# Optimization experiments

Measured on AMD Instinct MI355X. Metric: run time of the kernel, lower is better.

Reference implementation:

```python
import jax, jax.numpy as jnp
import numpy as np

N_NODES = 100000
N_EDGES = 1600000
IN_DIM = 128
HEADS = 4
OUT_DIM = 32
NEG_SLOPE = 0.2  # PyG GATConv default negative_slope


def setup_inputs() -> dict:
    key = jax.random.key(0)
    k_x, k_e, k_w, k_as, k_ad = jax.random.split(key, 5)
    x = jax.random.normal(k_x, (N_NODES, IN_DIM), dtype=jnp.float32)
    edge_index = jax.random.randint(k_e, (2, N_EDGES), 0, N_NODES, dtype=jnp.int64)
    # Glorot-style init for learned parameters (GATConv lin + attention vectors)
    W = jax.random.normal(k_w, (IN_DIM, HEADS * OUT_DIM), dtype=jnp.float32) / np.sqrt(IN_DIM)
    att_src = jax.random.normal(k_as, (HEADS, OUT_DIM), dtype=jnp.float32) / np.sqrt(OUT_DIM)
    att_dst = jax.random.normal(k_ad, (HEADS, OUT_DIM), dtype=jnp.float32) / np.sqrt(OUT_DIM)
    bias = jnp.zeros((HEADS * OUT_DIM,), dtype=jnp.float32)
    return {"x": x, "edge_index": edge_index, "W": W, "att_src": att_src,
            "att_dst": att_dst, "bias": bias}


def reference(x, edge_index, W, att_src, att_dst, bias):
    N = x.shape[0]
    H, D = att_src.shape
    # PyG GATConv default: add self loops
    loop = jnp.arange(N, dtype=edge_index.dtype)
    src = jnp.concatenate([edge_index[0], loop])  # message sources  [E+N]
    dst = jnp.concatenate([edge_index[1], loop])  # message targets  [E+N]

    h = (x @ W).reshape(N, H, D)                          # [N, H, D]
    a_src = jnp.einsum('nhd,hd->nh', h, att_src)          # [N, H]
    a_dst = jnp.einsum('nhd,hd->nh', h, att_dst)          # [N, H]

    # per-edge attention logits, LeakyReLU(neg_slope=0.2)
    e = jax.nn.leaky_relu(a_src[src] + a_dst[dst], NEG_SLOPE)  # [E+N, H]

    # segment softmax over edges grouped by target node (numerically stable)
    e_max = jax.ops.segment_max(e, dst, num_segments=N)        # [N, H]
    e_max = jnp.where(jnp.isfinite(e_max), e_max, jnp.float32(0))
    ex = jnp.exp(e - e_max[dst])                               # [E+N, H]
    denom = jax.ops.segment_sum(ex, dst, num_segments=N)       # [N, H]
    alpha = ex / (denom[dst] + jnp.float32(1e-16))             # [E+N, H]

    # weighted scatter-aggregate of source features
    msg = h[src] * alpha[:, :, None]                           # [E+N, H, D]
    out = jax.ops.segment_sum(msg, dst, num_segments=N)        # [N, H, D]
    out = out.reshape(N, H * D) + bias                         # concat heads + bias
    return jax.nn.elu(out)                                     # wrapper ELU
```

## Files before the change

kernel.cpp:

```cpp
#include <hip/hip_runtime.h>
#include <hip/hip_fp16.h>
#include <math.h>

#define N_NODES 100000
#define N_EDGES 1600000
#define IN_DIM 128
#define F_DIM 128
#define NEG_SLOPE 0.2f

#define BUCKW_LOG 7
#define NBUCK 784
#define NBLK 128
#define EPB 12500
#define G_TOT (NBUCK * NBLK)
#define SC_CHUNK 4096
#define SC_NB ((G_TOT + SC_CHUNK - 1) / SC_CHUNK)
#define CSR_CAP (N_EDGES + NBUCK * 384)
#define PADBIT 0x80000000u

typedef short v8s __attribute__((ext_vector_type(8)));
typedef float v4f __attribute__((ext_vector_type(4)));

static __device__ __forceinline__ unsigned short f2bf(float f) {
    unsigned u = __float_as_uint(f);
    u += 0x7fffu + ((u >> 16) & 1u);
    return (unsigned short)(u >> 16);
}
static __device__ __forceinline__ float lo2f(unsigned u) { return __uint_as_float(u << 16); }
static __device__ __forceinline__ float hi2f(unsigned u) { return __uint_as_float(u & 0xffff0000u); }

__global__ __launch_bounds__(256) void k_wprep(const float* __restrict__ W,
                                               unsigned short* __restrict__ Wt) {
    int i = blockIdx.x * 256 + threadIdx.x;
    int n = i >> 7, k = i & 127;
    Wt[n * 128 + k] = f2bf(W[k * 128 + n]);
}

__global__ __launch_bounds__(256) void k_gemm(const float* __restrict__ x,
                                              const unsigned short* __restrict__ Wt,
                                              unsigned short* __restrict__ h16,
                                              const float* __restrict__ att_src,
                                              const float* __restrict__ att_dst,
                                              float* __restrict__ a_src,
                                              float* __restrict__ a_dst) {
    __shared__ unsigned short As[64][136];
    __shared__ unsigned short Bs[128][136];
    __shared__ float attl[256];
    const int t  = threadIdx.x;
    const int n0 = blockIdx.x * 64;

    attl[t] = (t < 128) ? att_src[t] : att_dst[t - 128];

    {
        int row = t >> 2, k0 = (t & 3) * 32;
        int n = n0 + row;
        #pragma unroll
        for (int i = 0; i < 4; i++) {
            float4 va = make_float4(0.f,0.f,0.f,0.f), vb = va;
            if (n < N_NODES) {
                const float* p = x + (size_t)n * IN_DIM + k0 + i * 8;
                va = *(const float4*)p;
                vb = *(const float4*)(p + 4);
            }
            uint4 u;
            u.x = f2bf(va.x) | ((unsigned)f2bf(va.y) << 16);
            u.y = f2bf(va.z) | ((unsigned)f2bf(va.w) << 16);
            u.z = f2bf(vb.x) | ((unsigned)f2bf(vb.y) << 16);
            u.w = f2bf(vb.z) | ((unsigned)f2bf(vb.w) << 16);
            *(uint4*)&As[row][k0 + i * 8] = u;
        }
    }
    {
        int nr = t >> 1, s0 = (t & 1) * 64;
        const uint4* src = (const uint4*)(Wt + nr * 128 + s0);
        #pragma unroll
        for (int i = 0; i < 8; i++)
            *(uint4*)&Bs[nr][s0 + i * 8] = src[i];
    }
    __syncthreads();

    const int w = t >> 6, lane = t & 63;
    const int mr = lane & 15, quad = lane >> 4;
    const int m0 = w * 16;

    v4f acc[8];
    #pragma unroll
    for (int nt = 0; nt < 8; nt++) acc[nt] = (v4f){0.f, 0.f, 0.f, 0.f};

    #pragma unroll
    for (int kk = 0; kk < 4; kk++) {
        int kof = kk * 32 + quad * 8;
        v8s a = *(const v8s*)&As[m0 + mr][kof];
        #pragma unroll
        for (int nt = 0; nt < 8; nt++) {
            v8s b = *(const v8s*)&Bs[nt * 16 + mr][kof];
            acc[nt] = __builtin_amdgcn_mfma_f32_16x16x32_bf16(a, b, acc[nt], 0, 0, 0);
        }
    }

    #pragma unroll
    for (int nt = 0; nt < 8; nt++)
        #pragma unroll
        for (int r = 0; r < 4; r++)
            As[m0 + quad * 4 + r][nt * 16 + mr] = f2bf(acc[nt][r]);
    __syncthreads();
    {
        int row = m0 + (lane >> 2);
        int c0  = (lane & 3) * 32;
        int n = n0 + row;
        if (n < N_NODES) {
            float ds = 0.f, dd = 0.f;
            #pragma unroll
            for (int i = 0; i < 4; i++) {
                uint4 v = *(const uint4*)&As[row][c0 + i * 8];
                *(uint4*)&h16[(size_t)n * F_DIM + c0 + i * 8] = v;
                float f0 = lo2f(v.x), f1 = hi2f(v.x);
                float f2 = lo2f(v.y), f3 = hi2f(v.y);
                float f4 = lo2f(v.z), f5 = hi2f(v.z);
                float f6 = lo2f(v.w), f7 = hi2f(v.w);
                const float* ps = &attl[c0 + i * 8];
                const float* pd = &attl[128 + c0 + i * 8];
                ds += f0*ps[0] + f1*ps[1] + f2*ps[2] + f3*ps[3]
                    + f4*ps[4] + f5*ps[5] + f6*ps[6] + f7*ps[7];
                dd += f0*pd[0] + f1*pd[1] + f2*pd[2] + f3*pd[3]
                    + f4*pd[4] + f5*pd[5] + f6*pd[6] + f7*pd[7];
            }
            int hd = lane & 3;
            a_src[n * 4 + hd] = ds;
            a_dst[n * 4 + hd] = dd;
        }
    }
}

__global__ __launch_bounds__(1024) void k_bhist(const int* __restrict__ ei_dst,
                                                int* __restrict__ G) {
    __shared__ int hist[NBUCK];
    for (int i = threadIdx.x; i < NBUCK; i += 1024) hist[i] = 0;
    __syncthreads();
    const int4* p = (const int4*)(ei_dst + blockIdx.x * EPB);
    const int n4 = EPB / 4;
    for (int i = threadIdx.x; i < n4; i += 1024) {
        int4 d = p[i];
        atomicAdd(&hist[d.x >> BUCKW_LOG], 1);
        atomicAdd(&hist[d.y >> BUCKW_LOG], 1);
        atomicAdd(&hist[d.z >> BUCKW_LOG], 1);
        atomicAdd(&hist[d.w >> BUCKW_LOG], 1);
    }
    __syncthreads();
    for (int b = threadIdx.x; b < NBUCK; b += 1024)
        G[b * NBLK + blockIdx.x] = hist[b];
}

__global__ __launch_bounds__(256) void k_scanp(const int* __restrict__ a,
                                               int* __restrict__ part) {
    int base = blockIdx.x * SC_CHUNK + threadIdx.x * 16;
    int s = 0;
    #pragma unroll
    for (int i = 0; i < 16; i++) {
        int idx = base + i;
        if (idx < G_TOT) s += a[idx];
    }
    __shared__ int wsum[4];
    for (int off = 32; off >= 1; off >>= 1) s += __shfl_down(s, off, 64);
    if ((threadIdx.x & 63) == 0) wsum[threadIdx.x >> 6] = s;
    __syncthreads();
    if (threadIdx.x == 0) part[blockIdx.x] = wsum[0] + wsum[1] + wsum[2] + wsum[3];
}

__global__ void k_scant(int* part, int* boff) {
    int lane = threadIdx.x & 63;
    int v = (lane < SC_NB) ? part[lane] : 0;
    int x = v;
    #pragma unroll
    for (int off = 1; off < 64; off <<= 1) {
        int y = __shfl_up(x, off, 64);
        if (lane >= off) x += y;
    }
    if (lane < SC_NB) part[lane] = x - v;
    if (lane == 0) boff[NBUCK] = N_EDGES;
}

__global__ __launch_bounds__(256) void k_scand(int* __restrict__ a,
                                               const int* __restrict__ part,
                                               int* __restrict__ boff) {
    __shared__ int tsum[256];
    int tid  = threadIdx.x;
    int base = blockIdx.x * SC_CHUNK + tid * 16;
    int v[16]; int s = 0;
    #pragma unroll
    for (int i = 0; i < 16; i++) {
        int idx = base + i;
        v[i] = (idx < G_TOT) ? a[idx] : 0;
        s += v[i];
    }
    tsum[tid] = s;
    __syncthreads();
    for (int off = 1; off < 256; off <<= 1) {
        int y = (tid >= off) ? tsum[tid - off] : 0;
        __syncthreads();
        tsum[tid] += y;
        __syncthreads();
    }
    int run = part[blockIdx.x] + tsum[tid] - s;
    #pragma unroll
    for (int i = 0; i < 16; i++) {
        int idx = base + i;
        if (idx < G_TOT) {
            a[idx] = run;
            if (idx % NBLK == 0) boff[idx / NBLK] = run;
        }
        run += v[i];
    }
}

__global__ __launch_bounds__(1024) void k_bscat(const int* __restrict__ ei,
                                                const int* __restrict__ G,
                                                int* __restrict__ ebuf) {
    __shared__ int base[NBUCK];
    for (int b = threadIdx.x; b < NBUCK; b += 1024)
        base[b] = G[b * NBLK + blockIdx.x];
    __syncthreads();
    const int4* ps = (const int4*)(ei + blockIdx.x * EPB);
    const int4* pd = (const int4*)(ei + N_EDGES + blockIdx.x * EPB);
    const int n4 = EPB / 4;
    for (int i = threadIdx.x; i < n4; i += 1024) {
        int4 s = ps[i];
        int4 d = pd[i];
        int b0 = d.x >> BUCKW_LOG; int p0 = atomicAdd(&base[b0], 1);
        ebuf[p0] = s.x | ((d.x & 127) << 17);
        int b1 = d.y >> BUCKW_LOG; int p1 = atomicAdd(&base[b1], 1);
        ebuf[p1] = s.y | ((d.y & 127) << 17);
        int b2 = d.z >> BUCKW_LOG; int p2 = atomicAdd(&base[b2], 1);
        ebuf[p2] = s.z | ((d.z & 127) << 17);
        int b3 = d.w >> BUCKW_LOG; int p3 = atomicAdd(&base[b3], 1);
        ebuf[p3] = s.w | ((d.w & 127) << 17);
    }
}

__global__ __launch_bounds__(512) void k_csrfin(const int* __restrict__ ebuf,
                                                const int* __restrict__ boff,
                                                int2* __restrict__ ebounds,
                                                int* __restrict__ csr2) {
    __shared__ int cnt[128];
    __shared__ int off[128];
    __shared__ int wtot;
    int b = blockIdx.x;
    int beg = boff[b], end = boff[b + 1];
    int padded_base = beg + b * 384;
    int tid = threadIdx.x;
    if (tid < 128) cnt[tid] = 0;
    __syncthreads();
    {
        int j = beg + tid;
        for (; j + 3 * 512 < end; j += 4 * 512) {
            int e0 = ebuf[j];
            int e1 = ebuf[j + 512];
            int e2 = ebuf[j + 1024];
            int e3 = ebuf[j + 1536];
            atomicAdd(&cnt[(e0 >> 17) & 127], 1);
            atomicAdd(&cnt[(e1 >> 17) & 127], 1);
            atomicAdd(&cnt[(e2 >> 17) & 127], 1);
            atomicAdd(&cnt[(e3 >> 17) & 127], 1);
        }
        for (; j < end; j += 512)
            atomicAdd(&cnt[(ebuf[j] >> 17) & 127], 1);
    }
    __syncthreads();
    if (tid < 128) {
        int cp = (cnt[tid] + 3) & ~3;
        int x = cp;
        #pragma unroll
        for (int o = 1; o < 64; o <<= 1) {
            int y = __shfl_up(x, o, 64);
            if ((tid & 63) >= o) x += y;
        }
        off[tid] = x - cp;
        if (tid == 63) wtot = x;
    }
    __syncthreads();
    if (tid < 128) {
        int v = off[tid] + ((tid >= 64) ? wtot : 0) + padded_base;
        off[tid] = v;
        int node = (b << BUCKW_LOG) + tid;
        int c = cnt[tid];
        if (node < N_NODES) {
            ebounds[node] = make_int2(v, v + c);
            int cpad = (c + 3) & ~3;
            for (int k = c; k < cpad; k++)
                csr2[v + k] = node | PADBIT;
        }
        cnt[tid] = 0;
    }
    __syncthreads();
    {
        int j = beg + tid;
        for (; j + 3 * 512 < end; j += 4 * 512) {
            int e0 = ebuf[j];
            int e1 = ebuf[j + 512];
            int e2 = ebuf[j + 1024];
            int e3 = ebuf[j + 1536];
            int d0 = (e0 >> 17) & 127; int r0 = atomicAdd(&cnt[d0], 1);
            csr2[off[d0] + r0] = e0 & 0x1ffff;
            int d1 = (e1 >> 17) & 127; int r1 = atomicAdd(&cnt[d1], 1);
            csr2[off[d1] + r1] = e1 & 0x1ffff;
            int d2 = (e2 >> 17) & 127; int r2 = atomicAdd(&cnt[d2], 1);
            csr2[off[d2] + r2] = e2 & 0x1ffff;
            int d3 = (e3 >> 17) & 127; int r3 = atomicAdd(&cnt[d3], 1);
            csr2[off[d3] + r3] = e3 & 0x1ffff;
        }
        for (; j < end; j += 512) {
            int e0 = ebuf[j];
            int d0 = (e0 >> 17) & 127; int r0 = atomicAdd(&cnt[d0], 1);
            csr2[off[d0] + r0] = e0 & 0x1ffff;
        }
    }
}

__global__ __launch_bounds__(256) void k_agg(const uint4* __restrict__ h16x4,
                                             const float* __restrict__ a_src,
                                             const float* __restrict__ a_dst,
                                             const int2* __restrict__ ebounds,
                                             const int* __restrict__ csr2,
                                             const float* __restrict__ bias,
                                             float* __restrict__ out) {
    int n = (blockIdx.x * 256 + threadIdx.x) >> 6;
    if (n >= N_NODES) return;
    int lane = threadIdx.x & 63;
    int grp = lane >> 4, g = lane & 15, hd = g >> 2;

    float adn = a_dst[n * 4 + hd];
    float p0 = 0.f;
    if (grp == 0) {
        float e0 = a_src[n * 4 + hd] + adn;
        e0 = e0 > 0.f ? e0 : NEG_SLOPE * e0;
        p0 = __expf(e0);
    }
    uint4 hs = h16x4[(size_t)n * 16 + g];
    float l  = p0;
    float a0 = p0 * lo2f(hs.x), a1 = p0 * hi2f(hs.x);
    float a2 = p0 * lo2f(hs.y), a3 = p0 * hi2f(hs.y);
    float a4 = p0 * lo2f(hs.z), a5 = p0 * hi2f(hs.z);
    float a6 = p0 * lo2f(hs.w), a7 = p0 * hi2f(hs.w);

    int2 eb = ebounds[n];
    int beg = eb.x, cnt = eb.y - eb.x;
    const int* sp = csr2 + beg + grp;
    int steps = (cnt + 3) >> 2;
    int t = 0;
    for (; t + 2 <= steps; t += 2) {
        int u0 = sp[4 * t];
        int u1 = sp[4 * t + 4];
        int s0 = u0 & 0x7fffffff;
        int s1 = u1 & 0x7fffffff;
        float w0 = a_src[s0 * 4 + hd] + adn;
        float w1 = a_src[s1 * 4 + hd] + adn;
        uint4 h0 = h16x4[(size_t)s0 * 16 + g];
        uint4 h1 = h16x4[(size_t)s1 * 16 + g];
        w0 = w0 > 0.f ? w0 : NEG_SLOPE * w0;
        w1 = w1 > 0.f ? w1 : NEG_SLOPE * w1;
        float q0 = __expf(w0);
        float q1 = __expf(w1);
        q0 = u0 < 0 ? 0.f : q0;
        q1 = u1 < 0 ? 0.f : q1;
        l  += q0 + q1;
        a0 += q0 * lo2f(h0.x) + q1 * lo2f(h1.x);
        a1 += q0 * hi2f(h0.x) + q1 * hi2f(h1.x);
        a2 += q0 * lo2f(h0.y) + q1 * lo2f(h1.y);
        a3 += q0 * hi2f(h0.y) + q1 * hi2f(h1.y);
        a4 += q0 * lo2f(h0.z) + q1 * lo2f(h1.z);
        a5 += q0 * hi2f(h0.z) + q1 * hi2f(h1.z);
        a6 += q0 * lo2f(h0.w) + q1 * lo2f(h1.w);
        a7 += q0 * hi2f(h0.w) + q1 * hi2f(h1.w);
    }
    if (t < steps) {
        int u0 = sp[4 * t];
        int s0 = u0 & 0x7fffffff;
        float w0 = a_src[s0 * 4 + hd] + adn;
        uint4 h0 = h16x4[(size_t)s0 * 16 + g];
        w0 = w0 > 0.f ? w0 : NEG_SLOPE * w0;
        float q0 = __expf(w0);
        q0 = u0 < 0 ? 0.f : q0;
        l  += q0;
        a0 += q0 * lo2f(h0.x);
        a1 += q0 * hi2f(h0.x);
        a2 += q0 * lo2f(h0.y);
        a3 += q0 * hi2f(h0.y);
        a4 += q0 * lo2f(h0.z);
        a5 += q0 * hi2f(h0.z);
        a6 += q0 * lo2f(h0.w);
        a7 += q0 * hi2f(h0.w);
    }
    #define RED2(v) v += __shfl_xor(v, 16, 64); v += __shfl_xor(v, 32, 64);
    RED2(l); RED2(a0); RED2(a1); RED2(a2); RED2(a3);
    RED2(a4); RED2(a5); RED2(a6); RED2(a7);
    #undef RED2

    if (grp == 0) {
        float inv = 1.f / (l + 1e-16f);
        float4 b0 = *(const float4*)&bias[g * 8];
        float4 b1 = *(const float4*)&bias[g * 8 + 4];
        float o0 = a0 * inv + b0.x, o1 = a1 * inv + b0.y;
        float o2 = a2 * inv + b0.z, o3 = a3 * inv + b0.w;
        float o4 = a4 * inv + b1.x, o5 = a5 * inv + b1.y;
        float o6 = a6 * inv + b1.z, o7 = a7 * inv + b1.w;
        o0 = o0 > 0.f ? o0 : __expf(o0) - 1.f;
        o1 = o1 > 0.f ? o1 : __expf(o1) - 1.f;
        o2 = o2 > 0.f ? o2 : __expf(o2) - 1.f;
        o3 = o3 > 0.f ? o3 : __expf(o3) - 1.f;
        o4 = o4 > 0.f ? o4 : __expf(o4) - 1.f;
        o5 = o5 > 0.f ? o5 : __expf(o5) - 1.f;
        o6 = o6 > 0.f ? o6 : __expf(o6) - 1.f;
        o7 = o7 > 0.f ? o7 : __expf(o7) - 1.f;
        *(float4*)&out[(size_t)n * F_DIM + g * 8]     = make_float4(o0, o1, o2, o3);
        *(float4*)&out[(size_t)n * F_DIM + g * 8 + 4] = make_float4(o4, o5, o6, o7);
    }
}

extern "C" void kernel_launch(void* const* d_in, const int* in_sizes, int n_in,
                              void* d_out, int out_size, void* d_ws, size_t ws_size,
                              hipStream_t stream) {
    const float* x       = (const float*)d_in[0];
    const int*   ei      = (const int*)d_in[1];
    const float* W       = (const float*)d_in[2];
    const float* att_src = (const float*)d_in[3];
    const float* att_dst = (const float*)d_in[4];
    const float* bias    = (const float*)d_in[5];
    float*       out     = (float*)d_out;

    char* ws = (char*)d_ws;
    unsigned short* h16 = (unsigned short*)ws; ws += (size_t)N_NODES * F_DIM * 2;
    unsigned short* Wt  = (unsigned short*)ws; ws += (size_t)IN_DIM * F_DIM * 2;
    float* a_src  = (float*)ws; ws += (size_t)N_NODES * 4 * 4;
    float* a_dst  = (float*)ws; ws += (size_t)N_NODES * 4 * 4;
    int*   G      = (int*)ws;   ws += (size_t)G_TOT * 4;
    int*   part   = (int*)ws;   ws += 1024;
    int*   boff   = (int*)ws;   ws += 4096;
    int2*  ebounds= (int2*)ws;  ws += (size_t)N_NODES * 8 + 512;
    int*   ebuf   = (int*)ws;   ws += (size_t)N_EDGES * 4;
    int*   csr2   = (int*)ws;   ws += (size_t)CSR_CAP * 4;

    k_wprep<<<64, 256, 0, stream>>>(W, Wt);
    k_gemm<<<(N_NODES + 63) / 64, 256, 0, stream>>>(x, Wt, h16, att_src, att_dst, a_src, a_dst);

    k_bhist<<<NBLK, 1024, 0, stream>>>(ei + N_EDGES, G);
    k_scanp<<<SC_NB, 256, 0, stream>>>(G, part);
    k_scant<<<1, 64, 0, stream>>>(part, boff);
    k_scand<<<SC_NB, 256, 0, stream>>>(G, part, boff);
    k_bscat<<<NBLK, 1024, 0, stream>>>(ei, G, ebuf);
    k_csrfin<<<NBUCK, 512, 0, stream>>>(ebuf, boff, ebounds, csr2);

    k_agg<<<(N_NODES * 64 + 255) / 256, 256, 0, stream>>>((const uint4*)h16, a_src, a_dst, ebounds, csr2, bias, out);
}
```

Baseline: 255.4 us.

## Merge GEMM with bucket scatter and fold W prep into histogram kernel

```diff
diff --git a/kernel.cpp b/kernel.cpp
--- a/kernel.cpp
+++ b/kernel.cpp
@@ -17,6 +17,7 @@
 #define SC_NB ((G_TOT + SC_CHUNK - 1) / SC_CHUNK)
 #define CSR_CAP (N_EDGES + NBUCK * 384)
 #define PADBIT 0x80000000u
+#define GB 1563
 
 typedef short v8s __attribute__((ext_vector_type(8)));
 typedef float v4f __attribute__((ext_vector_type(4)));
@@ -29,20 +30,127 @@
 static __device__ __forceinline__ float lo2f(unsigned u) { return __uint_as_float(u << 16); }
 static __device__ __forceinline__ float hi2f(unsigned u) { return __uint_as_float(u & 0xffff0000u); }
 
-__global__ __launch_bounds__(256) void k_wprep(const float* __restrict__ W,
-                                               unsigned short* __restrict__ Wt) {
-    int i = blockIdx.x * 256 + threadIdx.x;
-    int n = i >> 7, k = i & 127;
-    Wt[n * 128 + k] = f2bf(W[k * 128 + n]);
-}
-
-__global__ __launch_bounds__(256) void k_gemm(const float* __restrict__ x,
+__global__ __launch_bounds__(1024) void k_bhist(const int* __restrict__ ei_dst,
+                                                int* __restrict__ G,
+                                                const float* __restrict__ W,
+                                                unsigned short* __restrict__ Wt) {
+    if (blockIdx.x < 16) {
+        int i = blockIdx.x * 1024 + threadIdx.x;
+        int n = i >> 7, k = i & 127;
+        Wt[n * 128 + k] = f2bf(W[k * 128 + n]);
+    }
+    __shared__ int hist[NBUCK];
+    for (int i = threadIdx.x; i < NBUCK; i += 1024) hist[i] = 0;
+    __syncthreads();
+    const int4* p = (const int4*)(ei_dst + blockIdx.x * EPB);
+    const int n4 = EPB / 4;
+    for (int i = threadIdx.x; i < n4; i += 1024) {
+        int4 d = p[i];
+        atomicAdd(&hist[d.x >> BUCKW_LOG], 1);
+        atomicAdd(&hist[d.y >> BUCKW_LOG], 1);
+        atomicAdd(&hist[d.z >> BUCKW_LOG], 1);
+        atomicAdd(&hist[d.w >> BUCKW_LOG], 1);
+    }
+    __syncthreads();
+    for (int b = threadIdx.x; b < NBUCK; b += 1024)
+        G[b * NBLK + blockIdx.x] = hist[b];
+}
+
+__global__ __launch_bounds__(256) void k_scanp(const int* __restrict__ a,
+                                               int* __restrict__ part) {
+    int base = blockIdx.x * SC_CHUNK + threadIdx.x * 16;
+    int s = 0;
+    #pragma unroll
+    for (int i = 0; i < 16; i++) {
+        int idx = base + i;
+        if (idx < G_TOT) s += a[idx];
+    }
+    __shared__ int wsum[4];
+    for (int off = 32; off >= 1; off >>= 1) s += __shfl_down(s, off, 64);
+    if ((threadIdx.x & 63) == 0) wsum[threadIdx.x >> 6] = s;
+    __syncthreads();
+    if (threadIdx.x == 0) part[blockIdx.x] = wsum[0] + wsum[1] + wsum[2] + wsum[3];
+}
+
+__global__ void k_scant(int* part, int* boff) {
+    int lane = threadIdx.x & 63;
+    int v = (lane < SC_NB) ? part[lane] : 0;
+    int x = v;
+    #pragma unroll
+    for (int off = 1; off < 64; off <<= 1) {
+        int y = __shfl_up(x, off, 64);
+        if (lane >= off) x += y;
+    }
+    if (lane < SC_NB) part[lane] = x - v;
+    if (lane == 0) boff[NBUCK] = N_EDGES;
+}
+
+__global__ __launch_bounds__(256) void k_scand(int* __restrict__ a,
+                                               const int* __restrict__ part,
+                                               int* __restrict__ boff) {
+    __shared__ int tsum[256];
+    int tid  = threadIdx.x;
+    int base = blockIdx.x * SC_CHUNK + tid * 16;
+    int v[16]; int s = 0;
+    #pragma unroll
+    for (int i = 0; i < 16; i++) {
+        int idx = base + i;
+        v[i] = (idx < G_TOT) ? a[idx] : 0;
+        s += v[i];
+    }
+    tsum[tid] = s;
+    __syncthreads();
+    for (int off = 1; off < 256; off <<= 1) {
+        int y = (tid >= off) ? tsum[tid - off] : 0;
+        __syncthreads();
+        tsum[tid] += y;
+        __syncthreads();
+    }
+    int run = part[blockIdx.x] + tsum[tid] - s;
+    #pragma unroll
+    for (int i = 0; i < 16; i++) {
+        int idx = base + i;
+        if (idx < G_TOT) {
+            a[idx] = run;
+            if (idx % NBLK == 0) boff[idx / NBLK] = run;
+        }
+        run += v[i];
+    }
+}
+
+__global__ __launch_bounds__(256) void k_mega(const float* __restrict__ x,
                                               const unsigned short* __restrict__ Wt,
                                               unsigned short* __restrict__ h16,
                                               const float* __restrict__ att_src,
                                               const float* __restrict__ att_dst,
                                               float* __restrict__ a_src,
-                                              float* __restrict__ a_dst) {
+                                              float* __restrict__ a_dst,
+                                              const int* __restrict__ ei,
+                                              const int* __restrict__ G,
+                                              int* __restrict__ ebuf) {
+    if (blockIdx.x >= GB) {
+        int blk = blockIdx.x - GB;
+        __shared__ int base[NBUCK];
+        for (int b = threadIdx.x; b < NBUCK; b += 256)
+            base[b] = G[b * NBLK + blk];
+        __syncthreads();
+        const int4* ps = (const int4*)(ei + blk * EPB);
+        const int4* pd = (const int4*)(ei + N_EDGES + blk * EPB);
+        for (int i = threadIdx.x; i < EPB / 4; i += 256) {
+            int4 s = ps[i];
+            int4 d = pd[i];
+            int b0 = d.x >> BUCKW_LOG; int p0 = atomicAdd(&base[b0], 1);
+            ebuf[p0] = s.x | ((d.x & 127) << 17);
+            int b1 = d.y >> BUCKW_LOG; int p1 = atomicAdd(&base[b1], 1);
+            ebuf[p1] = s.y | ((d.y & 127) << 17);
+            int b2 = d.z >> BUCKW_LOG; int p2 = atomicAdd(&base[b2], 1);
+            ebuf[p2] = s.z | ((d.z & 127) << 17);
+            int b3 = d.w >> BUCKW_LOG; int p3 = atomicAdd(&base[b3], 1);
+            ebuf[p3] = s.w | ((d.w & 127) << 17);
+        }
+        return;
+    }
+
     __shared__ unsigned short As[64][136];
     __shared__ unsigned short Bs[128][136];
     __shared__ float attl[256];
@@ -132,111 +240,6 @@
     }
 }
 
-__global__ __launch_bounds__(1024) void k_bhist(const int* __restrict__ ei_dst,
-                                                int* __restrict__ G) {
-    __shared__ int hist[NBUCK];
-    for (int i = threadIdx.x; i < NBUCK; i += 1024) hist[i] = 0;
-    __syncthreads();
-    const int4* p = (const int4*)(ei_dst + blockIdx.x * EPB);
-    const int n4 = EPB / 4;
-    for (int i = threadIdx.x; i < n4; i += 1024) {
-        int4 d = p[i];
-        atomicAdd(&hist[d.x >> BUCKW_LOG], 1);
-        atomicAdd(&hist[d.y >> BUCKW_LOG], 1);
-        atomicAdd(&hist[d.z >> BUCKW_LOG], 1);
-        atomicAdd(&hist[d.w >> BUCKW_LOG], 1);
-    }
-    __syncthreads();
-    for (int b = threadIdx.x; b < NBUCK; b += 1024)
-        G[b * NBLK + blockIdx.x] = hist[b];
-}
-
-__global__ __launch_bounds__(256) void k_scanp(const int* __restrict__ a,
-                                               int* __restrict__ part) {
-    int base = blockIdx.x * SC_CHUNK + threadIdx.x * 16;
-    int s = 0;
-    #pragma unroll
-    for (int i = 0; i < 16; i++) {
-        int idx = base + i;
-        if (idx < G_TOT) s += a[idx];
-    }
-    __shared__ int wsum[4];
-    for (int off = 32; off >= 1; off >>= 1) s += __shfl_down(s, off, 64);
-    if ((threadIdx.x & 63) == 0) wsum[threadIdx.x >> 6] = s;
-    __syncthreads();
-    if (threadIdx.x == 0) part[blockIdx.x] = wsum[0] + wsum[1] + wsum[2] + wsum[3];
-}
-
-__global__ void k_scant(int* part, int* boff) {
-    int lane = threadIdx.x & 63;
-    int v = (lane < SC_NB) ? part[lane] : 0;
-    int x = v;
-    #pragma unroll
-    for (int off = 1; off < 64; off <<= 1) {
-        int y = __shfl_up(x, off, 64);
-        if (lane >= off) x += y;
-    }
-    if (lane < SC_NB) part[lane] = x - v;
-    if (lane == 0) boff[NBUCK] = N_EDGES;
-}
-
-__global__ __launch_bounds__(256) void k_scand(int* __restrict__ a,
-                                               const int* __restrict__ part,
-                                               int* __restrict__ boff) {
-    __shared__ int tsum[256];
-    int tid  = threadIdx.x;
-    int base = blockIdx.x * SC_CHUNK + tid * 16;
-    int v[16]; int s = 0;
-    #pragma unroll
-    for (int i = 0; i < 16; i++) {
-        int idx = base + i;
-        v[i] = (idx < G_TOT) ? a[idx] : 0;
-        s += v[i];
-    }
-    tsum[tid] = s;
-    __syncthreads();
-    for (int off = 1; off < 256; off <<= 1) {
-        int y = (tid >= off) ? tsum[tid - off] : 0;
-        __syncthreads();
-        tsum[tid] += y;
-        __syncthreads();
-    }
-    int run = part[blockIdx.x] + tsum[tid] - s;
-    #pragma unroll
-    for (int i = 0; i < 16; i++) {
-        int idx = base + i;
-        if (idx < G_TOT) {
-            a[idx] = run;
-            if (idx % NBLK == 0) boff[idx / NBLK] = run;
-        }
-        run += v[i];
-    }
-}
-
-__global__ __launch_bounds__(1024) void k_bscat(const int* __restrict__ ei,
-                                                const int* __restrict__ G,
-                                                int* __restrict__ ebuf) {
-    __shared__ int base[NBUCK];
-    for (int b = threadIdx.x; b < NBUCK; b += 1024)
-        base[b] = G[b * NBLK + blockIdx.x];
-    __syncthreads();
-    const int4* ps = (const int4*)(ei + blockIdx.x * EPB);
-    const int4* pd = (const int4*)(ei + N_EDGES + blockIdx.x * EPB);
-    const int n4 = EPB / 4;
-    for (int i = threadIdx.x; i < n4; i += 1024) {
-        int4 s = ps[i];
-        int4 d = pd[i];
-        int b0 = d.x >> BUCKW_LOG; int p0 = atomicAdd(&base[b0], 1);
-        ebuf[p0] = s.x | ((d.x & 127) << 17);
-        int b1 = d.y >> BUCKW_LOG; int p1 = atomicAdd(&base[b1], 1);
-        ebuf[p1] = s.y | ((d.y & 127) << 17);
-        int b2 = d.z >> BUCKW_LOG; int p2 = atomicAdd(&base[b2], 1);
-        ebuf[p2] = s.z | ((d.z & 127) << 17);
-        int b3 = d.w >> BUCKW_LOG; int p3 = atomicAdd(&base[b3], 1);
-        ebuf[p3] = s.w | ((d.w & 127) << 17);
-    }
-}
-
 __global__ __launch_bounds__(512) void k_csrfin(const int* __restrict__ ebuf,
                                                 const int* __restrict__ boff,
                                                 int2* __restrict__ ebounds,
@@ -346,22 +349,26 @@
     int beg = eb.x, cnt = eb.y - eb.x;
     const int* sp = csr2 + beg + grp;
     int steps = (cnt + 3) >> 2;
+    int u0 = (steps > 0) ? sp[0] : 0;
+    int u1 = (steps > 1) ? sp[4] : 0;
     int t = 0;
     for (; t + 2 <= steps; t += 2) {
-        int u0 = sp[4 * t];
-        int u1 = sp[4 * t + 4];
         int s0 = u0 & 0x7fffffff;
         int s1 = u1 & 0x7fffffff;
-        float w0 = a_src[s0 * 4 + hd] + adn;
-        float w1 = a_src[s1 * 4 + hd] + adn;
+        int m0 = u0, m1 = u1;
+        float as0 = a_src[s0 * 4 + hd];
+        float as1 = a_src[s1 * 4 + hd];
         uint4 h0 = h16x4[(size_t)s0 * 16 + g];
         uint4 h1 = h16x4[(size_t)s1 * 16 + g];
-        w0 = w0 > 0.f ? w0 : NEG_SLOPE * w0;
-        w1 = w1 > 0.f ? w1 : NEG_SLOPE * w1;
+        int tn = t + 2;
+        u0 = (tn < steps) ? sp[4 * tn] : 0;
+        u1 = (tn + 1 < steps) ? sp[4 * tn + 4] : 0;
+        float w0 = as0 + adn; w0 = w0 > 0.f ? w0 : NEG_SLOPE * w0;
+        float w1 = as1 + adn; w1 = w1 > 0.f ? w1 : NEG_SLOPE * w1;
         float q0 = __expf(w0);
         float q1 = __expf(w1);
-        q0 = u0 < 0 ? 0.f : q0;
-        q1 = u1 < 0 ? 0.f : q1;
+        q0 = m0 < 0 ? 0.f : q0;
+        q1 = m1 < 0 ? 0.f : q1;
         l  += q0 + q1;
         a0 += q0 * lo2f(h0.x) + q1 * lo2f(h1.x);
         a1 += q0 * hi2f(h0.x) + q1 * hi2f(h1.x);
@@ -373,13 +380,13 @@
         a7 += q0 * hi2f(h0.w) + q1 * hi2f(h1.w);
     }
     if (t < steps) {
-        int u0 = sp[4 * t];
         int s0 = u0 & 0x7fffffff;
-        float w0 = a_src[s0 * 4 + hd] + adn;
+        int m0 = u0;
+        float as0 = a_src[s0 * 4 + hd];
         uint4 h0 = h16x4[(size_t)s0 * 16 + g];
-        w0 = w0 > 0.f ? w0 : NEG_SLOPE * w0;
+        float w0 = as0 + adn; w0 = w0 > 0.f ? w0 : NEG_SLOPE * w0;
         float q0 = __expf(w0);
-        q0 = u0 < 0 ? 0.f : q0;
+        q0 = m0 < 0 ? 0.f : q0;
         l  += q0;
         a0 += q0 * lo2f(h0.x);
         a1 += q0 * hi2f(h0.x);
@@ -439,14 +446,12 @@
     int*   ebuf   = (int*)ws;   ws += (size_t)N_EDGES * 4;
     int*   csr2   = (int*)ws;   ws += (size_t)CSR_CAP * 4;
 
-    k_wprep<<<64, 256, 0, stream>>>(W, Wt);
-    k_gemm<<<(N_NODES + 63) / 64, 256, 0, stream>>>(x, Wt, h16, att_src, att_dst, a_src, a_dst);
-
-    k_bhist<<<NBLK, 1024, 0, stream>>>(ei + N_EDGES, G);
+    k_bhist<<<NBLK, 1024, 0, stream>>>(ei + N_EDGES, G, W, Wt);
     k_scanp<<<SC_NB, 256, 0, stream>>>(G, part);
     k_scant<<<1, 64, 0, stream>>>(part, boff);
     k_scand<<<SC_NB, 256, 0, stream>>>(G, part, boff);
-    k_bscat<<<NBLK, 1024, 0, stream>>>(ei, G, ebuf);
+    k_mega<<<GB + NBLK, 256, 0, stream>>>(x, Wt, h16, att_src, att_dst,
+                                          a_src, a_dst, ei, G, ebuf);
     k_csrfin<<<NBUCK, 512, 0, stream>>>(ebuf, boff, ebounds, csr2);
 
     k_agg<<<(N_NODES * 64 + 255) / 256, 256, 0, stream>>>((const uint4*)h16, a_src, a_dst, ebounds, csr2, bias, out);
```

After: 260.9 us. 2.2% more time.
